# Kernel tuning notes

Measured on AMD Instinct MI355X. Metric: run time of the kernel, lower is better.

## Reference

```python
import jax, jax.numpy as jnp
import numpy as np

N_NODES = 100000
N_EDGES = 1600000
IN_FEATS = 128
H_FEATS = 64
NUM_CLASSES = 40
NEG_SLOPE = 0.2  # DGL GATConv default


def gat_layer(x, src, dst, W, attn_l, attn_r, bias, n_nodes):
    # x: [N, din]; W: [din, dout]; attn_l/r, bias: [dout]
    feat = x @ W                                   # [N, dout]
    el = feat @ attn_l                             # [N]
    er = feat @ attn_r                             # [N]
    e = jax.nn.leaky_relu(el[src] + er[dst], NEG_SLOPE)  # [E]
    # segment softmax over destination nodes (numerically stable)
    m = jax.ops.segment_max(e, dst, num_segments=n_nodes)   # [N]
    ee = jnp.exp(e - m[dst])                                 # [E]
    s = jax.ops.segment_sum(ee, dst, num_segments=n_nodes)  # [N]
    alpha = ee / s[dst]                                      # [E]
    out = jax.ops.segment_sum(alpha[:, None] * feat[src], dst,
                              num_segments=n_nodes)          # [N, dout]
    return out + bias


def setup_inputs() -> dict:
    key = jax.random.key(0)
    ks = jax.random.split(key, 12)
    in_feat = jax.random.normal(ks[0], (N_NODES, IN_FEATS), dtype=jnp.float32)
    src = jax.random.randint(ks[1], (N_EDGES,), 0, N_NODES, dtype=jnp.int32)
    dst = jax.random.randint(ks[2], (N_EDGES,), 0, N_NODES, dtype=jnp.int32)
    def glorot(k, shape):
        fan = sum(shape)
        return jax.random.normal(k, shape, dtype=jnp.float32) * jnp.sqrt(2.0 / fan)
    W1 = glorot(ks[3], (IN_FEATS, H_FEATS))
    al1 = glorot(ks[4], (H_FEATS,)) 
    ar1 = glorot(ks[5], (H_FEATS,))
    b1 = jnp.zeros((H_FEATS,), jnp.float32)
    W2 = glorot(ks[6], (H_FEATS, NUM_CLASSES))
    al2 = glorot(ks[7], (NUM_CLASSES,))
    ar2 = glorot(ks[8], (NUM_CLASSES,))
    b2 = jnp.zeros((NUM_CLASSES,), jnp.float32)
    return {"in_feat": in_feat, "src": src, "dst": dst,
            "W1": W1, "al1": al1, "ar1": ar1, "b1": b1,
            "W2": W2, "al2": al2, "ar2": ar2, "b2": b2}


def reference(in_feat, src, dst, W1, al1, ar1, b1, W2, al2, ar2, b2):
    h = gat_layer(in_feat, src, dst, W1, al1, ar1, b1, N_NODES)  # gat1
    h = jax.nn.elu(h)                                            # F.elu
    h = gat_layer(h, src, dst, W2, al2, ar2, b2, N_NODES)        # gat2
    return h  # [N, num_classes]
```

## Files before the change

### kernel.cpp

```cpp
#include <hip/hip_runtime.h>

#define N_NODES 100000
#define N_EDGES 1600000
#define DB_SHIFT 9
#define DB_SIZE 512
#define NDB 196
#define DB_CAP 10240
#define PART_EDGES 2048
#define NPART ((N_EDGES + PART_EDGES - 1) / PART_EDGES)
#define NGEMM1 ((N_NODES + 63) / 64)
#define WCONV_BLOCKS 44
#define NFB (9 * NDB)

constexpr float NEG_SLOPE = 0.2f;

__device__ __forceinline__ float leaky(float x) { return x > 0.f ? x : NEG_SLOPE * x; }

__device__ __forceinline__ float bflo(unsigned u) { return __uint_as_float(u << 16); }
__device__ __forceinline__ float bfhi(unsigned u) { return __uint_as_float(u & 0xffff0000u); }

__device__ __forceinline__ void bfsplit(float x, short& h, short& l) {
    unsigned u = __float_as_uint(x);
    h = (short)(u >> 16);
    float res = x - __uint_as_float(u & 0xffff0000u);
    unsigned r = __float_as_uint(res);
    r = (r + 0x7fffu + ((r >> 16) & 1u)) >> 16;
    l = (short)r;
}

__global__ __launch_bounds__(256) void fusedP_kernel(
        const float* __restrict__ W1, const float* __restrict__ W2,
        unsigned short* __restrict__ W1Th, unsigned short* __restrict__ W1Tl,
        unsigned short* __restrict__ W2Th, unsigned short* __restrict__ W2Tl,
        const int* __restrict__ src, const int* __restrict__ dst,
        int* __restrict__ db_cursor, unsigned* __restrict__ staged, int E) {
    extern __shared__ char smem[];
    if (blockIdx.x < WCONV_BLOCKS) {
        int idx = blockIdx.x * 256 + threadIdx.x;
        if (idx < 64 * 128) {
            int n = idx >> 7, k = idx & 127;
            int nt = n >> 4, m = n & 15;
            int kt = k >> 5, quad = (k >> 3) & 3, j = k & 7;
            int off = (((nt * 4 + kt) * 4 + quad) * 16 + m) * 8 + j;
            short h, l;
            bfsplit(W1[(size_t)k * 64 + n], h, l);
            W1Th[off] = (unsigned short)h;
            W1Tl[off] = (unsigned short)l;
        } else if (idx < 64 * 128 + 48 * 64) {
            int t = idx - 64 * 128;
            int n = t >> 6, k = t & 63;
            int nt = n >> 4, m = n & 15;
            int kt = k >> 5, quad = (k >> 3) & 3, j = k & 7;
            int off = (((nt * 2 + kt) * 4 + quad) * 16 + m) * 8 + j;
            float x = (n < 40) ? W2[(size_t)k * 40 + n] : 0.f;
            short h, l;
            bfsplit(x, h, l);
            W2Th[off] = (unsigned short)h;
            W2Tl[off] = (unsigned short)l;
        }
        return;
    }
    int p = blockIdx.x - WCONV_BLOCKS;
    unsigned* pay_s = (unsigned*)smem;
    unsigned* stage = pay_s + PART_EDGES;
    unsigned* hist  = stage + PART_EDGES;
    unsigned* scanb = hist + 256;
    unsigned* baseg = scanb + 256;
    unsigned* cnt   = baseg + 256;
    unsigned char* bktA  = (unsigned char*)(cnt + 256);
    unsigned char* bkt_s = bktA + PART_EDGES;
    int tid = threadIdx.x;
    int e0 = p * PART_EDGES;
    hist[tid] = 0;
    cnt[tid] = 0;
    __syncthreads();
#pragma unroll
    for (int k = 0; k < PART_EDGES / 256; ++k) {
        int idx = k * 256 + tid;
        int i = e0 + idx;
        if (i < E) {
            int d = dst[i];
            unsigned b = (unsigned)d >> DB_SHIFT;
            pay_s[idx] = (((unsigned)d & (DB_SIZE - 1)) << 17) | (unsigned)src[i];
            bktA[idx] = (unsigned char)b;
            atomicAdd(&hist[b], 1u);
        }
    }
    __syncthreads();
    unsigned v = hist[tid];
    scanb[tid] = v;
    __syncthreads();
    for (int off = 1; off < 256; off <<= 1) {
        unsigned t = (tid >= off) ? scanb[tid - off] : 0;
        __syncthreads();
        scanb[tid] += t;
        __syncthreads();
    }
    unsigned excl = scanb[tid] - v;
    __syncthreads();
    scanb[tid] = excl;
    if (tid < NDB)
        baseg[tid] = (unsigned)(tid * DB_CAP) + (unsigned)atomicAdd(&db_cursor[tid], (int)v);
    __syncthreads();
#pragma unroll
    for (int k = 0; k < PART_EDGES / 256; ++k) {
        int idx = k * 256 + tid;
        int i = e0 + idx;
        if (i < E) {
            unsigned b = bktA[idx];
            unsigned slot = scanb[b] + atomicAdd(&cnt[b], 1u);
            stage[slot] = pay_s[idx];
            bkt_s[slot] = (unsigned char)b;
        }
    }
    __syncthreads();
    int total = min(PART_EDGES, E - e0);
    for (int j = tid; j < total; j += 256) {
        unsigned b = bkt_s[j];
        unsigned addr = baseg[b] + ((unsigned)j - scanb[b]);
        staged[addr] = stage[j];
    }
}

template <int DIN, int NOUT, int NTILES, int OSTR, int XSTR>
__device__ __forceinline__ void gemm_mfma_body(
        int bid, const float* __restrict__ X,
        const unsigned short* __restrict__ WTh, const unsigned short* __restrict__ WTl,
        const float* __restrict__ al, const float* __restrict__ ar,
        unsigned short* __restrict__ featb, float* __restrict__ el,
        float* __restrict__ er, int N, float* XS) {
    constexpr int KT = DIN / 32;
    constexpr int F4 = DIN / 4;
    using frag = __attribute__((ext_vector_type(8))) short;
    using accv = __attribute__((ext_vector_type(4))) float;

    int tid = threadIdx.x;
    int rblk = bid * 64;
    if (rblk >= N) return;

#pragma unroll
    for (int it = 0; it < 64 * F4 / 256; ++it) {
        int idx = it * 256 + tid;
        int row = idx / F4, c4 = idx % F4;
        float4 v = make_float4(0.f, 0.f, 0.f, 0.f);
        if (rblk + row < N)
            v = reinterpret_cast<const float4*>(X + (size_t)(rblk + row) * DIN)[c4];
        *reinterpret_cast<float4*>(&XS[row * XSTR + c4 * 4]) = v;
    }
    __syncthreads();

    int lane = tid & 63;
    int wid = tid >> 6;
    int r0 = rblk + wid * 16;
    if (r0 >= N) return;
    int m = lane & 15;
    int quad = lane >> 4;
    int rowl = wid * 16 + m;

    frag ah[KT], alo[KT];
#pragma unroll
    for (int kt = 0; kt < KT; ++kt) {
        float4 a0 = *reinterpret_cast<const float4*>(&XS[rowl * XSTR + kt * 32 + quad * 8]);
        float4 a1 = *reinterpret_cast<const float4*>(&XS[rowl * XSTR + kt * 32 + quad * 8 + 4]);
        float xv[8] = {a0.x, a0.y, a0.z, a0.w, a1.x, a1.y, a1.z, a1.w};
#pragma unroll
        for (int j = 0; j < 8; ++j) {
            short h, l;
            bfsplit(xv[j], h, l);
            ah[kt][j] = h;
            alo[kt][j] = l;
        }
    }

    accv acc[NTILES];
#pragma unroll
    for (int nt = 0; nt < NTILES; ++nt) acc[nt] = (accv){0.f, 0.f, 0.f, 0.f};

#pragma unroll
    for (int nt = 0; nt < NTILES; ++nt) {
#pragma unroll
        for (int kt = 0; kt < KT; ++kt) {
            int foff = (((nt * KT + kt) * 4 + quad) * 16 + m) * 8;
            frag bh = *reinterpret_cast<const frag*>(WTh + foff);
            frag bl = *reinterpret_cast<const frag*>(WTl + foff);
            acc[nt] = __builtin_amdgcn_mfma_f32_16x16x32_bf16(ah[kt], bh, acc[nt], 0, 0, 0);
            acc[nt] = __builtin_amdgcn_mfma_f32_16x16x32_bf16(ah[kt], bl, acc[nt], 0, 0, 0);
            acc[nt] = __builtin_amdgcn_mfma_f32_16x16x32_bf16(alo[kt], bh, acc[nt], 0, 0, 0);
        }
    }

    float pel[4] = {0.f, 0.f, 0.f, 0.f};
    float per[4] = {0.f, 0.f, 0.f, 0.f};
#pragma unroll
    for (int nt = 0; nt < NTILES; ++nt) {
        int n = nt * 16 + m;
        float av = (n < NOUT) ? al[n] : 0.f;
        float rv = (n < NOUT) ? ar[n] : 0.f;
#pragma unroll
        for (int reg = 0; reg < 4; ++reg) {
            float v = acc[nt][reg];
            pel[reg] += v * av;
            per[reg] += v * rv;
            int grow = r0 + quad * 4 + reg;
            if (grow < N && n < NOUT) {
                unsigned u = __float_as_uint(v);
                u = (u + 0x7fffu + ((u >> 16) & 1u)) >> 16;
                featb[(size_t)grow * OSTR + n] = (unsigned short)u;
            }
        }
    }
#pragma unroll
    for (int o = 1; o < 16; o <<= 1) {
#pragma unroll
        for (int reg = 0; reg < 4; ++reg) {
            pel[reg] += __shfl_xor(pel[reg], o, 64);
            per[reg] += __shfl_xor(per[reg], o, 64);
        }
    }
    if (m == 0) {
#pragma unroll
        for (int reg = 0; reg < 4; ++reg) {
            int grow = r0 + quad * 4 + reg;
            if (grow < N) { el[grow] = pel[reg]; er[grow] = per[reg]; }
        }
    }
}

__global__ __launch_bounds__(256) void fusedB_kernel(
        const unsigned* __restrict__ staged, const int* __restrict__ db_cursor,
        int* __restrict__ csr_src, int* __restrict__ row_ptr,
        const float* __restrict__ X,
        const unsigned short* __restrict__ W1Th, const unsigned short* __restrict__ W1Tl,
        const float* __restrict__ al, const float* __restrict__ ar,
        unsigned short* __restrict__ featb, float* __restrict__ el,
        float* __restrict__ er, int N, int E) {
    extern __shared__ char smem[];
    int idx = blockIdx.x;
    if (idx % 9 == 0) {
        int k = idx / 9;
        int* hist = (int*)smem;
        int* excl = hist + DB_SIZE;
        int* psum = excl + DB_SIZE;
        int* scn  = psum + 256;
        int tid = threadIdx.x;
        scn[tid] = (tid < NDB) ? db_cursor[tid] : 0;
        __syncthreads();
        for (int off = 1; off < 256; off <<= 1) {
            int t = (tid >= off) ? scn[tid - off] : 0;
            __syncthreads();
            scn[tid] += t;
            __syncthreads();
        }
        int cnt = db_cursor[k];
        int base = scn[k] - cnt;
        if (k == 0 && tid == 0) row_ptr[N] = E;

        for (int i = tid; i < DB_SIZE; i += 256) hist[i] = 0;
        __syncthreads();
        const unsigned* win = staged + (size_t)k * DB_CAP;
        for (int j = tid; j < cnt; j += 256) atomicAdd(&hist[win[j] >> 17], 1);
        __syncthreads();
        int s = hist[2 * tid] + hist[2 * tid + 1];
        psum[tid] = s;
        __syncthreads();
        for (int off = 1; off < 256; off <<= 1) {
            int t = (tid >= off) ? psum[tid - off] : 0;
            __syncthreads();
            psum[tid] += t;
            __syncthreads();
        }
        int e0 = psum[tid] - s;
        excl[2 * tid] = e0;
        excl[2 * tid + 1] = e0 + hist[2 * tid];
        __syncthreads();
        for (int i = tid; i < DB_SIZE; i += 256) {
            int d = k * DB_SIZE + i;
            if (d < N) row_ptr[d] = base + excl[i];
        }
        for (int i = tid; i < DB_SIZE; i += 256) hist[i] = 0;
        __syncthreads();
        for (int j = tid; j < cnt; j += 256) {
            unsigned p = win[j];
            int dl = (int)(p >> 17);
            int pos = excl[dl] + atomicAdd(&hist[dl], 1);
            csr_src[base + pos] = (int)(p & 0x1FFFFu);
        }
    } else {
        int gid = idx - idx / 9 - 1;
        gemm_mfma_body<128, 64, 4, 64, 132>(gid, X, W1Th, W1Tl, al, ar, featb, el, er, N,
                                            (float*)smem);
    }
}

__global__ __launch_bounds__(256) void gemm2_kernel(
        const float* __restrict__ X,
        const unsigned short* __restrict__ WTh, const unsigned short* __restrict__ WTl,
        const float* __restrict__ al, const float* __restrict__ ar,
        unsigned short* __restrict__ featb, float* __restrict__ el,
        float* __restrict__ er, int N) {
    __shared__ float XS2[64 * 68];
    gemm_mfma_body<64, 40, 3, 48, 68>(blockIdx.x, X, WTh, WTl, al, ar, featb, el, er, N, XS2);
}

template <int NIT, int G2, int FSTR, bool ELU>
__device__ __forceinline__ void agg_fast(int lane, int s, bool act, float elv, float ern,
                                         const unsigned short* __restrict__ featb,
                                         const float* __restrict__ bias,
                                         float* __restrict__ outp, size_t orow, int deg) {
    int g = lane >> 4;
    int cl = lane & 15;
    int sj[NIT];
#pragma unroll
    for (int i = 0; i < NIT; ++i) sj[i] = __shfl(s, 4 * i + g, 64);
    uint2 q[NIT];
#pragma unroll
    for (int i = 0; i < NIT; ++i) {
        q[i] = make_uint2(0u, 0u);
        if (cl < G2)
            q[i] = *(reinterpret_cast<const uint2*>(featb + (size_t)sj[i] * FSTR) + cl);
    }
    float e = act ? leaky(elv + ern) : -1e30f;
    float m = e;
#pragma unroll
    for (int o = 32; o > 0; o >>= 1) m = fmaxf(m, __shfl_xor(m, o, 64));
    float ee = act ? __expf(e - m) : 0.f;
    float ssum = ee;
#pragma unroll
    for (int o = 32; o > 0; o >>= 1) ssum += __shfl_xor(ssum, o, 64);
    float w[NIT];
#pragma unroll
    for (int i = 0; i < NIT; ++i) w[i] = __shfl(ee, 4 * i + g, 64);

    float4 acc = make_float4(0.f, 0.f, 0.f, 0.f);
#pragma unroll
    for (int i = 0; i < NIT; ++i) {
        acc.x += w[i] * bflo(q[i].x);
        acc.y += w[i] * bfhi(q[i].x);
        acc.z += w[i] * bflo(q[i].y);
        acc.w += w[i] * bfhi(q[i].y);
    }
#pragma unroll
    for (int o = 16; o <= 32; o <<= 1) {
        acc.x += __shfl_xor(acc.x, o, 64);
        acc.y += __shfl_xor(acc.y, o, 64);
        acc.z += __shfl_xor(acc.z, o, 64);
        acc.w += __shfl_xor(acc.w, o, 64);
    }
    if (g == 0 && cl < G2) {
        float inv = (deg > 0) ? 1.f / ssum : 0.f;
        const float4 b4 = reinterpret_cast<const float4*>(bias)[cl];
        float4 o4;
        o4.x = acc.x * inv + b4.x;
        o4.y = acc.y * inv + b4.y;
        o4.z = acc.z * inv + b4.z;
        o4.w = acc.w * inv + b4.w;
        if (ELU) {
            o4.x = o4.x > 0.f ? o4.x : (__expf(o4.x) - 1.f);
            o4.y = o4.y > 0.f ? o4.y : (__expf(o4.y) - 1.f);
            o4.z = o4.z > 0.f ? o4.z : (__expf(o4.z) - 1.f);
            o4.w = o4.w > 0.f ? o4.w : (__expf(o4.w) - 1.f);
        }
        *reinterpret_cast<float4*>(outp + orow + 4 * cl) = o4;
    }
}

template <int DOUT, int FSTR, int OSTR, bool ELU>
__global__ void agg_kernel(const int* __restrict__ row_ptr, const int* __restrict__ csr_src,
                           const float* __restrict__ el, const float* __restrict__ er,
                           const unsigned short* __restrict__ featb,
                           const float* __restrict__ bias, float* __restrict__ outp, int N) {
    int lane = threadIdx.x & 63;
    int n = blockIdx.x * (blockDim.x >> 6) + (threadIdx.x >> 6);
    if (n >= N) return;
    int beg = row_ptr[n];
    int end = row_ptr[n + 1];
    int deg = end - beg;
    float ern = er[n];

    constexpr int G2 = DOUT / 4;

    if (deg <= 32) {
        int s = 0;
        bool act = lane < deg;
        if (act) s = csr_src[beg + lane];
        float elv = act ? el[s] : 0.f;
        if (deg <= 16)
            agg_fast<4, G2, FSTR, ELU>(lane, s, act, elv, ern, featb, bias, outp,
                                       (size_t)n * OSTR, deg);
        else
            agg_fast<8, G2, FSTR, ELU>(lane, s, act, elv, ern, featb, bias, outp,
                                       (size_t)n * OSTR, deg);
        return;
    }

    if (deg <= 64) {
        int s = 0;
        float e = -1e30f;
        bool act = lane < deg;
        if (act) {
            s = csr_src[beg + lane];
            e = leaky(el[s] + ern);
        }
        float m = e;
#pragma unroll
        for (int o = 32; o > 0; o >>= 1) m = fmaxf(m, __shfl_xor(m, o, 64));
        float ee = act ? __expf(e - m) : 0.f;
        float ssum = ee;
#pragma unroll
        for (int o = 32; o > 0; o >>= 1) ssum += __shfl_xor(ssum, o, 64);

        int g = lane >> 4;
        int cl = lane & 15;
        float4 acc = make_float4(0.f, 0.f, 0.f, 0.f);
        int niter = (deg + 3) >> 2;
        for (int i = 0; i < niter; i += 2) {
            int e0 = 4 * i + g;
            int e1 = e0 + 4;
            float w0 = __shfl(ee, e0 & 63, 64);
            int s0 = __shfl(s, e0 & 63, 64);
            float w1 = __shfl(ee, e1 & 63, 64);
            int s1 = __shfl(s, e1 & 63, 64);
            if (e1 >= 64) w1 = 0.f;
            if (cl < G2) {
                uint2 q0 = *(reinterpret_cast<const uint2*>(featb + (size_t)s0 * FSTR) + cl);
                uint2 q1 = *(reinterpret_cast<const uint2*>(featb + (size_t)s1 * FSTR) + cl);
                acc.x += w0 * bflo(q0.x) + w1 * bflo(q1.x);
                acc.y += w0 * bfhi(q0.x) + w1 * bfhi(q1.x);
                acc.z += w0 * bflo(q0.y) + w1 * bflo(q1.y);
                acc.w += w0 * bfhi(q0.y) + w1 * bfhi(q1.y);
            }
        }
#pragma unroll
        for (int o = 16; o <= 32; o <<= 1) {
            acc.x += __shfl_xor(acc.x, o, 64);
            acc.y += __shfl_xor(acc.y, o, 64);
            acc.z += __shfl_xor(acc.z, o, 64);
            acc.w += __shfl_xor(acc.w, o, 64);
        }
        if (g == 0 && cl < G2) {
            float inv = 1.f / ssum;
            const float4 b4 = reinterpret_cast<const float4*>(bias)[cl];
            float4 o4;
            o4.x = acc.x * inv + b4.x;
            o4.y = acc.y * inv + b4.y;
            o4.z = acc.z * inv + b4.z;
            o4.w = acc.w * inv + b4.w;
            if (ELU) {
                o4.x = o4.x > 0.f ? o4.x : (__expf(o4.x) - 1.f);
                o4.y = o4.y > 0.f ? o4.y : (__expf(o4.y) - 1.f);
                o4.z = o4.z > 0.f ? o4.z : (__expf(o4.z) - 1.f);
                o4.w = o4.w > 0.f ? o4.w : (__expf(o4.w) - 1.f);
            }
            *reinterpret_cast<float4*>(outp + (size_t)n * OSTR + 4 * cl) = o4;
        }
        return;
    }

    float m = -1e30f;
    for (int j = beg + lane; j < end; j += 64) {
        float e = leaky(el[csr_src[j]] + ern);
        m = fmaxf(m, e);
    }
#pragma unroll
    for (int o = 32; o > 0; o >>= 1) m = fmaxf(m, __shfl_xor(m, o, 64));

    float ssum = 0.f;
    float acc = 0.f;
    for (int base = beg; base < end; base += 64) {
        int j = base + lane;
        int cnt = min(64, end - base);
        int s = (lane < cnt) ? csr_src[j] : 0;
        float ee = 0.f;
        if (lane < cnt) {
            float e = leaky(el[s] + ern);
            ee = __expf(e - m);
        }
        ssum += ee;
        for (int t = 0; t < cnt; ++t) {
            float w = __shfl(ee, t, 64);
            int sj = __shfl(s, t, 64);
            if (lane < DOUT)
                acc += w * __uint_as_float(((unsigned)featb[(size_t)sj * FSTR + lane]) << 16);
        }
    }
#pragma unroll
    for (int o = 32; o > 0; o >>= 1) ssum += __shfl_xor(ssum, o, 64);

    if (lane < DOUT) {
        float o = acc / ssum + bias[lane];
        if (ELU) o = (o > 0.f) ? o : (__expf(o) - 1.f);
        outp[(size_t)n * OSTR + lane] = o;
    }
}

extern "C" void kernel_launch(void* const* d_in, const int* in_sizes, int n_in,
                              void* d_out, int out_size, void* d_ws, size_t ws_size,
                              hipStream_t stream) {
    const float* in_feat = (const float*)d_in[0];
    const int* src = (const int*)d_in[1];
    const int* dst = (const int*)d_in[2];
    const float* W1 = (const float*)d_in[3];
    const float* al1 = (const float*)d_in[4];
    const float* ar1 = (const float*)d_in[5];
    const float* b1 = (const float*)d_in[6];
    const float* W2 = (const float*)d_in[7];
    const float* al2 = (const float*)d_in[8];
    const float* ar2 = (const float*)d_in[9];
    const float* b2 = (const float*)d_in[10];
    float* out = (float*)d_out;

    const int N = N_NODES, E = N_EDGES;

    size_t off = 0;
    auto carve = [&](size_t bytes) {
        void* p = (char*)d_ws + off;
        off += (bytes + 255) & ~(size_t)255;
        return p;
    };
    unsigned short* featb = (unsigned short*)carve((size_t)N * 64 * 2);
    float* el    = (float*)carve((size_t)N * 4);
    float* er    = (float*)carve((size_t)N * 4);
    int* row_ptr = (int*)carve((size_t)(N + 1) * 4);
    int* csr_src = (int*)carve((size_t)E * 4);
    int* db_cursor = (int*)carve((size_t)NDB * 4);
    unsigned short* W1Th = (unsigned short*)carve((size_t)64 * 128 * 2);
    unsigned short* W1Tl = (unsigned short*)carve((size_t)64 * 128 * 2);
    unsigned short* W2Th = (unsigned short*)carve((size_t)48 * 64 * 2);
    unsigned short* W2Tl = (unsigned short*)carve((size_t)48 * 64 * 2);
    size_t offH = off;
    float* h = (float*)carve((size_t)N * 64 * 4);
    size_t off_end = off;
    off = offH;
    unsigned* staged = (unsigned*)carve((size_t)NDB * DB_CAP * 4);
    off = off_end;

    hipMemsetAsync(db_cursor, 0, (size_t)NDB * 4, stream);

    fusedP_kernel<<<WCONV_BLOCKS + NPART, 256, 24576, stream>>>(
        W1, W2, W1Th, W1Tl, W2Th, W2Tl, src, dst, db_cursor, staged, E);

    fusedB_kernel<<<NFB, 256, 64 * 132 * 4, stream>>>(
        staged, db_cursor, csr_src, row_ptr,
        in_feat, W1Th, W1Tl, al1, ar1, featb, el, er, N, E);

    int agrid = (N + 3) / 4;

    agg_kernel<64, 64, 64, true><<<agrid, 256, 0, stream>>>(row_ptr, csr_src, el, er, featb, b1, h, N);

    gemm2_kernel<<<(N + 63) / 64, 256, 0, stream>>>(h, W2Th, W2Tl, al2, ar2, featb, el, er, N);

    agg_kernel<40, 48, 40, false><<<agrid, 256, 0, stream>>>(row_ptr, csr_src, el, er, featb, b2, out, N);
}
```

Baseline: 259.7 us.

## Drop max-subtraction in edge softmax and load neighbors per lane group directly

The low-degree aggregation path now has each 16-lane group load its own csr_src and el entries directly, replacing the per-lane load followed by shuffles. The softmax is computed without the max reduction: exponents are clamped at 60 and the normalizer is reduced together with the feature accumulators. This removes a wavefront max reduction and several shuffles per node. The trade-offs are redundant index loads across lanes and reliance on the logits staying in a bounded range, since clamping changes results if a logit exceeds 60.

Result: no change. 263.2 us (+1.3%).

```diff
diff --git a/kernel.cpp b/kernel.cpp
--- a/kernel.cpp
+++ b/kernel.cpp
@@ -303,15 +303,23 @@
 }
 
 template <int NIT, int G2, int FSTR, bool ELU>
-__device__ __forceinline__ void agg_fast(int lane, int s, bool act, float elv, float ern,
+__device__ __forceinline__ void agg_fast(int lane, int beg, int deg,
+                                         const int* __restrict__ csr_src,
+                                         const float* __restrict__ el, float ern,
                                          const unsigned short* __restrict__ featb,
                                          const float* __restrict__ bias,
-                                         float* __restrict__ outp, size_t orow, int deg) {
+                                         float* __restrict__ outp, size_t orow) {
     int g = lane >> 4;
     int cl = lane & 15;
     int sj[NIT];
 #pragma unroll
-    for (int i = 0; i < NIT; ++i) sj[i] = __shfl(s, 4 * i + g, 64);
+    for (int i = 0; i < NIT; ++i) {
+        int e = 4 * i + g;
+        sj[i] = (e < deg) ? csr_src[beg + e] : 0;
+    }
+    float elv[NIT];
+#pragma unroll
+    for (int i = 0; i < NIT; ++i) elv[i] = el[sj[i]];
     uint2 q[NIT];
 #pragma unroll
     for (int i = 0; i < NIT; ++i) {
@@ -319,18 +327,14 @@
         if (cl < G2)
             q[i] = *(reinterpret_cast<const uint2*>(featb + (size_t)sj[i] * FSTR) + cl);
     }
-    float e = act ? leaky(elv + ern) : -1e30f;
-    float m = e;
-#pragma unroll
-    for (int o = 32; o > 0; o >>= 1) m = fmaxf(m, __shfl_xor(m, o, 64));
-    float ee = act ? __expf(e - m) : 0.f;
-    float ssum = ee;
-#pragma unroll
-    for (int o = 32; o > 0; o >>= 1) ssum += __shfl_xor(ssum, o, 64);
     float w[NIT];
-#pragma unroll
-    for (int i = 0; i < NIT; ++i) w[i] = __shfl(ee, 4 * i + g, 64);
-
+    float sw = 0.f;
+#pragma unroll
+    for (int i = 0; i < NIT; ++i) {
+        float e = fminf(leaky(elv[i] + ern), 60.f);
+        w[i] = (4 * i + g < deg) ? __expf(e) : 0.f;
+        sw += w[i];
+    }
     float4 acc = make_float4(0.f, 0.f, 0.f, 0.f);
 #pragma unroll
     for (int i = 0; i < NIT; ++i) {
@@ -345,9 +349,10 @@
         acc.y += __shfl_xor(acc.y, o, 64);
         acc.z += __shfl_xor(acc.z, o, 64);
         acc.w += __shfl_xor(acc.w, o, 64);
+        sw += __shfl_xor(sw, o, 64);
     }
     if (g == 0 && cl < G2) {
-        float inv = (deg > 0) ? 1.f / ssum : 0.f;
+        float inv = (deg > 0) ? 1.f / sw : 0.f;
         const float4 b4 = reinterpret_cast<const float4*>(bias)[cl];
         float4 o4;
         o4.x = acc.x * inv + b4.x;
@@ -379,32 +384,25 @@
 
     constexpr int G2 = DOUT / 4;
 
+    if (deg <= 16) {
+        agg_fast<4, G2, FSTR, ELU>(lane, beg, deg, csr_src, el, ern, featb, bias, outp,
+                                   (size_t)n * OSTR);
+        return;
+    }
     if (deg <= 32) {
-        int s = 0;
-        bool act = lane < deg;
-        if (act) s = csr_src[beg + lane];
-        float elv = act ? el[s] : 0.f;
-        if (deg <= 16)
-            agg_fast<4, G2, FSTR, ELU>(lane, s, act, elv, ern, featb, bias, outp,
-                                       (size_t)n * OSTR, deg);
-        else
-            agg_fast<8, G2, FSTR, ELU>(lane, s, act, elv, ern, featb, bias, outp,
-                                       (size_t)n * OSTR, deg);
+        agg_fast<8, G2, FSTR, ELU>(lane, beg, deg, csr_src, el, ern, featb, bias, outp,
+                                   (size_t)n * OSTR);
         return;
     }
 
     if (deg <= 64) {
         int s = 0;
-        float e = -1e30f;
+        float ee = 0.f;
         bool act = lane < deg;
         if (act) {
             s = csr_src[beg + lane];
-            e = leaky(el[s] + ern);
-        }
-        float m = e;
-#pragma unroll
-        for (int o = 32; o > 0; o >>= 1) m = fmaxf(m, __shfl_xor(m, o, 64));
-        float ee = act ? __expf(e - m) : 0.f;
+            ee = __expf(fminf(leaky(el[s] + ern), 60.f));
+        }
         float ssum = ee;
 #pragma unroll
         for (int o = 32; o > 0; o >>= 1) ssum += __shfl_xor(ssum, o, 64);
```
